# Kernel optimization log

Measured on AMD Instinct MI355X. Metric: run time of the kernel, lower is better.

Reference implementation:

```python
import jax, jax.numpy as jnp
import numpy as np

EMBED_DIM = 1024


def setup_inputs() -> dict:
    key = jax.random.key(0)
    ks = jax.random.split(key, 9)
    B, S, D = 4, 4096, EMBED_DIM
    s = 1.0 / np.sqrt(D)
    inp = {"x": jax.random.normal(ks[0], (B, S, D), dtype=jnp.float32)}
    names = ["q", "k", "v", "out"]
    for i, n in enumerate(names):
        inp[f"w_{n}"] = jax.random.uniform(ks[1 + 2 * i], (D, D), jnp.float32, -s, s)
        inp[f"b_{n}"] = jax.random.uniform(ks[2 + 2 * i], (D,), jnp.float32, -s, s)
    return inp


def reference(x, w_q, b_q, w_k, b_k, w_v, b_v, w_out, b_out):
    D = x.shape[-1]
    scaling = 1.0 / jnp.sqrt(jnp.asarray(D, x.dtype))
    q = jnp.einsum("bsd,ed->bse", x, w_q) + b_q
    k = jnp.einsum("bsd,ed->bse", x, w_k) + b_k
    v = jnp.einsum("bsd,ed->bse", x, w_v) + b_v
    # full [B, S, S] attention matrix, as in the original module
    scores = jnp.einsum("bqd,bkd->bqk", q, k) * scaling
    attn = jax.nn.softmax(scores, axis=-1)
    out = jnp.einsum("bqk,bkd->bqd", attn, v)
    return jnp.einsum("bsd,ed->bse", out, w_out) + b_out
```

## Files before the change

kernel.cpp:

```cpp
#include <hip/hip_runtime.h>
#include <hip/hip_bf16.h>

typedef __hip_bfloat16 bf16;
typedef __bf16 bf16x8 __attribute__((ext_vector_type(8)));
typedef float f32x4 __attribute__((ext_vector_type(4)));

#define B_ 4
#define S_ 4096
#define D_ 1024
#define BS_ 16384
#define N3_ 3072

__device__ __forceinline__ void gld_lds16(const void* g, void* l) {
    __builtin_amdgcn_global_load_lds(
        (const __attribute__((address_space(1))) void*)g,
        (__attribute__((address_space(3))) void*)l, 16, 0, 0);
}

__device__ __forceinline__ void cast4_one(const float* __restrict__ in,
                                          bf16* __restrict__ out, int i) {
    float4 v = ((const float4*)in)[i];
    union { ushort4 u; bf16 h[4]; } cv;
    cv.h[0] = __float2bfloat16(v.x);
    cv.h[1] = __float2bfloat16(v.y);
    cv.h[2] = __float2bfloat16(v.z);
    cv.h[3] = __float2bfloat16(v.w);
    ((ushort4*)out)[i] = cv.u;
}

__global__ __launch_bounds__(256) void prologue(
    const float* __restrict__ x, const float* __restrict__ wq,
    const float* __restrict__ wk, const float* __restrict__ wv,
    const float* __restrict__ wo, const float* __restrict__ bq,
    const float* __restrict__ bk, const float* __restrict__ bv,
    bf16* __restrict__ xb, bf16* __restrict__ Wc, bf16* __restrict__ Wo,
    float* __restrict__ bc, float* __restrict__ ls) {
    const int blk = blockIdx.x, tid = threadIdx.x;
    if (blk < 16384) {
        cast4_one(x, xb, blk * 256 + tid);
    } else if (blk < 20480) {
        int w = (blk - 16384) >> 10;
        int i = ((blk - 16384) & 1023) * 256 + tid;
        const float* src = (w == 0) ? wq : (w == 1) ? wk : (w == 2) ? wv : wo;
        bf16* dst = (w == 3) ? Wo : Wc + (long)w * D_ * D_;
        cast4_one(src, dst, i);
    } else if (blk < 20544) {
        ls[(blk - 20480) * 256 + tid] = 0.f;
    } else {
        for (int i = tid; i < N3_; i += 256)
            bc[i] = (i < 1024) ? bq[i] : (i < 2048) ? bk[i - 1024] : bv[i - 2048];
    }
}

__global__ __launch_bounds__(256) void transpose_v(const bf16* __restrict__ QKV,
                                                   bf16* __restrict__ VT) {
    __shared__ bf16 t[32][33];
    const int b = blockIdx.z;
    const bf16* Vb = QKV + (long)b * S_ * N3_ + 2048;
    bf16* VTb = VT + (long)b * D_ * S_;
    const int s0 = blockIdx.x * 32, d0 = blockIdx.y * 32;
    const int r = threadIdx.x >> 5, c = threadIdx.x & 31;
#pragma unroll
    for (int i = 0; i < 4; i++)
        t[r + i * 8][c] = Vb[(long)(s0 + r + i * 8) * N3_ + d0 + c];
    __syncthreads();
#pragma unroll
    for (int i = 0; i < 4; i++)
        VTb[(long)(d0 + r + i * 8) * S_ + s0 + c] = t[c][r + i * 8];
}

template <int EPI, int BM>
__global__ __launch_bounds__(256, 2) void gemm_nt(
    const bf16* __restrict__ A, int lda, long sA,
    const bf16* __restrict__ B, int ldb, long sB,
    void* __restrict__ Cout, int ldc, long sC,
    int K, const float* __restrict__ bias,
    float* __restrict__ rowsum, int sL, float scale) {
    constexpr int MI = BM / 32;
    __shared__ __align__(16) bf16 As[BM * 64];
    __shared__ __align__(16) bf16 Bs[128 * 64];
    const int tid = threadIdx.x;
    const int lane = tid & 63;
    const int wave = tid >> 6;
    const int bz = blockIdx.z;
    const int m0 = blockIdx.x * BM, n0 = blockIdx.y * 128;
    A += (long)bz * sA;
    B += (long)bz * sB;
    rowsum += (long)bz * sL;

    const int wr = (wave >> 1) * (BM / 2);
    const int wc = (wave & 1) * 64;
    const int fm = lane & 15;
    const int q4 = lane >> 4;
    const int sw = fm & 7;
    const int rd0 = ((q4 ^ sw) << 3);
    const int rd1 = (((4 + q4) ^ sw) << 3);

    f32x4 zero = {0.f, 0.f, 0.f, 0.f};
    f32x4 acc[MI][4];
#pragma unroll
    for (int i = 0; i < MI; i++)
#pragma unroll
        for (int j = 0; j < 4; j++) acc[i][j] = zero;

    for (int k0 = 0; k0 < K; k0 += 64) {
#pragma unroll
        for (int t = 0; t < BM / 32; t++) {
            int c = tid + t * 256;
            int row = c >> 3;
            int q = (((c & 7) ^ (row & 7)) << 3);
            gld_lds16(A + (long)(m0 + row) * lda + k0 + q, As + c * 8);
        }
#pragma unroll
        for (int t = 0; t < 4; t++) {
            int c = tid + t * 256;
            int row = c >> 3;
            int q = (((c & 7) ^ (row & 7)) << 3);
            gld_lds16(B + (long)(n0 + row) * ldb + k0 + q, Bs + c * 8);
        }
        __syncthreads();
#pragma unroll
        for (int kh = 0; kh < 2; kh++) {
            const int rdo = kh ? rd1 : rd0;
            bf16x8 af[MI], bfr[4];
#pragma unroll
            for (int i = 0; i < MI; i++)
                af[i] = *(const bf16x8*)(As + (wr + i * 16 + fm) * 64 + rdo);
#pragma unroll
            for (int j = 0; j < 4; j++)
                bfr[j] = *(const bf16x8*)(Bs + (wc + j * 16 + fm) * 64 + rdo);
#pragma unroll
            for (int i = 0; i < MI; i++)
#pragma unroll
                for (int j = 0; j < 4; j++)
                    acc[i][j] = __builtin_amdgcn_mfma_f32_16x16x32_bf16(
                        af[i], bfr[j], acc[i][j], 0, 0, 0);
        }
        __syncthreads();
    }

#pragma unroll
    for (int i = 0; i < MI; i++)
#pragma unroll
        for (int r = 0; r < 4; r++) {
            const int grow = m0 + wr + q4 * 4 + i * 16 + r;
            if constexpr (EPI == 0) {
#pragma unroll
                for (int j = 0; j < 4; j++) {
                    int gcol = n0 + wc + j * 16 + fm;
                    ((bf16*)Cout)[(long)bz * sC + (long)grow * ldc + gcol] =
                        __float2bfloat16(acc[i][j][r] + bias[gcol]);
                }
            } else if constexpr (EPI == 1) {
                float s = 0.f;
#pragma unroll
                for (int j = 0; j < 4; j++) {
                    int gcol = n0 + wc + j * 16 + fm;
                    float v = __expf(acc[i][j][r] * scale);
                    bf16 hv = __float2bfloat16(v);
                    ((bf16*)Cout)[(long)bz * sC + (long)grow * ldc + gcol] = hv;
                    s += __bfloat162float(hv);
                }
                s += __shfl_xor(s, 1, 16);
                s += __shfl_xor(s, 2, 16);
                s += __shfl_xor(s, 4, 16);
                s += __shfl_xor(s, 8, 16);
                if (fm == 0) atomicAdd(rowsum + grow, s);
            } else if constexpr (EPI == 2) {
                float inv = 1.0f / rowsum[grow];
#pragma unroll
                for (int j = 0; j < 4; j++) {
                    int gcol = n0 + wc + j * 16 + fm;
                    ((bf16*)Cout)[(long)bz * sC + (long)grow * ldc + gcol] =
                        __float2bfloat16(acc[i][j][r] * inv);
                }
            } else {
#pragma unroll
                for (int j = 0; j < 4; j++) {
                    int gcol = n0 + wc + j * 16 + fm;
                    ((float*)Cout)[(long)bz * sC + (long)grow * ldc + gcol] =
                        acc[i][j][r] + bias[gcol];
                }
            }
        }
}

extern "C" void kernel_launch(void* const* d_in, const int* in_sizes, int n_in,
                              void* d_out, int out_size, void* d_ws, size_t ws_size,
                              hipStream_t stream) {
    const float* x  = (const float*)d_in[0];
    const float* wq = (const float*)d_in[1];
    const float* bq = (const float*)d_in[2];
    const float* wk = (const float*)d_in[3];
    const float* bk = (const float*)d_in[4];
    const float* wv = (const float*)d_in[5];
    const float* bv = (const float*)d_in[6];
    const float* wo = (const float*)d_in[7];
    const float* bo = (const float*)d_in[8];
    (void)in_sizes; (void)n_in; (void)out_size;

    char* p = (char*)d_ws;
    bf16* Wc  = (bf16*)p;  p += (long)N3_ * D_ * 2;
    bf16* Wo  = (bf16*)p;  p += (long)D_ * D_ * 2;
    float* bc = (float*)p; p += N3_ * 4;
    bf16* QKV = (bf16*)p;  p += (long)BS_ * N3_ * 2;
    float* ls = (float*)p; p += (long)BS_ * 4;

    bf16* xb = (bf16*)d_out;

    const size_t base = 109129728UL;
    int tier;
    bf16 *VT, *E;
    if (ws_size >= base + 134217728UL) {
        tier = 2;
        E  = (bf16*)p;
        VT = (bf16*)((char*)d_out + 33554432);
    } else if (ws_size >= base + 33554432UL) {
        tier = 1;
        VT = (bf16*)p;
        E  = (bf16*)d_out;
    } else {
        tier = 0;
        VT = (bf16*)((char*)d_out + 33554432);
        E  = (bf16*)d_out;
    }

    prologue<<<dim3(20545), 256, 0, stream>>>(x, wq, wk, wv, wo, bq, bk, bv,
                                              xb, Wc, Wo, bc, ls);

    gemm_nt<0, 128><<<dim3(BS_ / 128, N3_ / 128, 1), 256, 0, stream>>>(
        xb, D_, 0, Wc, D_, 0, QKV, N3_, 0, D_, bc, ls, 0, 1.f);

    transpose_v<<<dim3(S_ / 32, D_ / 32, B_), 256, 0, stream>>>(QKV, VT);

    if (tier == 2) {
        gemm_nt<1, 128><<<dim3(32, 32, 4), 256, 0, stream>>>(
            QKV, N3_, (long)S_ * N3_, QKV + 1024, N3_, (long)S_ * N3_,
            E, S_, (long)S_ * S_, D_, nullptr, ls, S_, 0.03125f);
        gemm_nt<2, 128><<<dim3(32, 8, 4), 256, 0, stream>>>(
            E, S_, (long)S_ * S_, VT, S_, (long)D_ * S_,
            QKV, N3_, (long)S_ * N3_, S_, nullptr, ls, S_, 1.f);
    } else if (tier == 1) {
        for (int pr = 0; pr < 2; ++pr) {
            const long qoff = (long)(2 * pr) * S_ * N3_;
            gemm_nt<1, 128><<<dim3(32, 32, 2), 256, 0, stream>>>(
                QKV + qoff, N3_, (long)S_ * N3_,
                QKV + qoff + 1024, N3_, (long)S_ * N3_,
                E, S_, (long)S_ * S_, D_, nullptr, ls + 2 * pr * S_, S_, 0.03125f);
            gemm_nt<2, 128><<<dim3(32, 8, 2), 256, 0, stream>>>(
                E, S_, (long)S_ * S_,
                VT + (long)(2 * pr) * D_ * S_, S_, (long)D_ * S_,
                QKV + qoff, N3_, (long)S_ * N3_, S_, nullptr, ls + 2 * pr * S_, S_, 1.f);
        }
    } else {
        for (int b = 0; b < B_; ++b) {
            const long qoff = (long)b * S_ * N3_;
            gemm_nt<1, 128><<<dim3(32, 32, 1), 256, 0, stream>>>(
                QKV + qoff, N3_, 0, QKV + qoff + 1024, N3_, 0,
                E, S_, 0, D_, nullptr, ls + b * S_, 0, 0.03125f);
            gemm_nt<2, 64><<<dim3(64, 8, 1), 256, 0, stream>>>(
                E, S_, 0, VT + (long)b * D_ * S_, S_, 0,
                QKV + qoff, N3_, 0, S_, nullptr, ls + b * S_, 0, 1.f);
        }
    }

    gemm_nt<3, 128><<<dim3(BS_ / 128, D_ / 128, 1), 256, 0, stream>>>(
        QKV, N3_, 0, Wo, D_, 0, d_out, D_, 0, D_, bo, ls, 0, 1.f);
}
```

Before: 589.4 us.

## Add 256x256-tile 8-wave GEMM with ping-pong LDS pipeline for all matmuls

Introduces a new GEMM kernel with 256x256 output tiles, 512 threads (8 waves), double-buffered LDS fed by direct global-to-LDS loads, and interleaved barriers with MFMA priority raising, similar to a ping-pong schedule. The QKV projection, the scores/exp GEMM, the PV GEMM (tier 2 path) and the output projection are switched to it. The larger tile raises arithmetic intensity per LDS/global load and is meant to overlap loads with MFMA work. In exchange it uses 128KB of LDS and heavy register pressure, launches fewer blocks (wave-quantization risk), and the tier 0/1 fallback paths still use the old kernel.

```diff
diff --git a/kernel.cpp b/kernel.cpp
--- a/kernel.cpp
+++ b/kernel.cpp
@@ -185,6 +185,182 @@
         }
 }
 
+__device__ __forceinline__ void stage_half(const bf16* __restrict__ g, int ld,
+                                           bf16* l, int tid) {
+#pragma unroll
+    for (int t = 0; t < 2; t++) {
+        const int ch = tid + t * 512;
+        gld_lds16(g + (long)(ch >> 2) * ld + ((ch & 3) << 3), l + ch * 8);
+    }
+    asm volatile("" ::: "memory");
+}
+
+__device__ __forceinline__ void ds_a4(bf16x8 (&d)[4], const bf16* base, int ro,
+                                      int wr, int fm, int q4) {
+#pragma unroll
+    for (int i = 0; i < 4; i++)
+        d[i] = *(const bf16x8*)(base + (wr + ro + i * 16 + fm) * 32 + (q4 << 3));
+}
+
+__device__ __forceinline__ void ds_b4(bf16x8 (&d)[4], const bf16* base,
+                                      int wc, int fm, int q4) {
+#pragma unroll
+    for (int j = 0; j < 4; j++)
+        d[j] = *(const bf16x8*)(base + (wc + j * 16 + fm) * 32 + (q4 << 3));
+}
+
+template <int IO>
+__device__ __forceinline__ void mfma16(f32x4 (&acc)[8][4], const bf16x8 (&a)[4],
+                                       const bf16x8 (&b)[4]) {
+    __builtin_amdgcn_s_setprio(1);
+#pragma unroll
+    for (int i = 0; i < 4; i++)
+#pragma unroll
+        for (int j = 0; j < 4; j++)
+            acc[IO + i][j] = __builtin_amdgcn_mfma_f32_16x16x32_bf16(
+                a[i], b[j], acc[IO + i][j], 0, 0, 0);
+    __builtin_amdgcn_s_setprio(0);
+}
+
+#define BAR() __builtin_amdgcn_s_barrier()
+#define LGKM0() asm volatile("s_waitcnt lgkmcnt(0)" ::: "memory")
+#define VM4() asm volatile("s_waitcnt vmcnt(4)" ::: "memory")
+#define VM0() asm volatile("s_waitcnt vmcnt(0)" ::: "memory")
+
+template <int EPI>
+__global__ __launch_bounds__(512, 2) void gemm8(
+    const bf16* __restrict__ A, int lda, long sA,
+    const bf16* __restrict__ B, int ldb, long sB,
+    void* __restrict__ Cout, int ldc, long sC,
+    int K, const float* __restrict__ bias,
+    float* __restrict__ rowsum, int sL, float scale) {
+    __shared__ __align__(16) bf16 As[2][2][256 * 32];
+    __shared__ __align__(16) bf16 Bs[2][2][256 * 32];
+    const int tid = threadIdx.x;
+    const int lane = tid & 63;
+    const int wave = tid >> 6;
+    const int bz = blockIdx.z;
+    const int m0 = blockIdx.x * 256, n0 = blockIdx.y * 256;
+    A += (long)bz * sA + (long)m0 * lda;
+    B += (long)bz * sB + (long)n0 * ldb;
+    rowsum += (long)bz * sL;
+
+    const int wm = wave >> 2, wn = wave & 3;
+    const int wr = wm * 128, wc = wn * 64;
+    const int fm = lane & 15, q4 = lane >> 4;
+
+    f32x4 zero = {0.f, 0.f, 0.f, 0.f};
+    f32x4 acc[8][4];
+#pragma unroll
+    for (int i = 0; i < 8; i++)
+#pragma unroll
+        for (int j = 0; j < 4; j++) acc[i][j] = zero;
+
+    const int NT = K >> 6;
+    stage_half(A, lda, &As[0][0][0], tid);
+    stage_half(B, ldb, &Bs[0][0][0], tid);
+    stage_half(A + 32, lda, &As[0][1][0], tid);
+    stage_half(B + 32, ldb, &Bs[0][1][0], tid);
+    VM4();
+    BAR();
+
+    bf16x8 a[4], b[4];
+    for (int t = 0; t + 1 < NT; ++t) {
+        const int c = t & 1, n = c ^ 1;
+        const int kn = (t + 1) << 6;
+        ds_a4(a, &As[c][0][0], 0, wr, fm, q4);
+        ds_b4(b, &Bs[c][0][0], wc, fm, q4);
+        stage_half(A + kn, lda, &As[n][0][0], tid);
+        BAR(); LGKM0();
+        mfma16<0>(acc, a, b);
+        BAR();
+        ds_a4(a, &As[c][0][0], 64, wr, fm, q4);
+        stage_half(B + kn, ldb, &Bs[n][0][0], tid);
+        BAR(); LGKM0();
+        mfma16<4>(acc, a, b);
+        VM4();
+        BAR();
+        ds_a4(a, &As[c][1][0], 0, wr, fm, q4);
+        ds_b4(b, &Bs[c][1][0], wc, fm, q4);
+        stage_half(A + kn + 32, lda, &As[n][1][0], tid);
+        BAR(); LGKM0();
+        mfma16<0>(acc, a, b);
+        BAR();
+        ds_a4(a, &As[c][1][0], 64, wr, fm, q4);
+        stage_half(B + kn + 32, ldb, &Bs[n][1][0], tid);
+        BAR(); LGKM0();
+        mfma16<4>(acc, a, b);
+        VM4();
+        BAR();
+    }
+    {
+        const int c = (NT - 1) & 1;
+        ds_a4(a, &As[c][0][0], 0, wr, fm, q4);
+        ds_b4(b, &Bs[c][0][0], wc, fm, q4);
+        BAR(); LGKM0();
+        mfma16<0>(acc, a, b);
+        BAR();
+        ds_a4(a, &As[c][0][0], 64, wr, fm, q4);
+        BAR(); LGKM0();
+        mfma16<4>(acc, a, b);
+        VM0();
+        BAR();
+        ds_a4(a, &As[c][1][0], 0, wr, fm, q4);
+        ds_b4(b, &Bs[c][1][0], wc, fm, q4);
+        BAR(); LGKM0();
+        mfma16<0>(acc, a, b);
+        BAR();
+        ds_a4(a, &As[c][1][0], 64, wr, fm, q4);
+        BAR(); LGKM0();
+        mfma16<4>(acc, a, b);
+    }
+
+#pragma unroll
+    for (int mi = 0; mi < 8; mi++)
+#pragma unroll
+        for (int r = 0; r < 4; r++) {
+            const int grow = m0 + wr + mi * 16 + q4 * 4 + r;
+            if constexpr (EPI == 0) {
+#pragma unroll
+                for (int j = 0; j < 4; j++) {
+                    int gcol = n0 + wc + j * 16 + fm;
+                    ((bf16*)Cout)[(long)bz * sC + (long)grow * ldc + gcol] =
+                        __float2bfloat16(acc[mi][j][r] + bias[gcol]);
+                }
+            } else if constexpr (EPI == 1) {
+                float s = 0.f;
+#pragma unroll
+                for (int j = 0; j < 4; j++) {
+                    int gcol = n0 + wc + j * 16 + fm;
+                    float v = __expf(acc[mi][j][r] * scale);
+                    bf16 hv = __float2bfloat16(v);
+                    ((bf16*)Cout)[(long)bz * sC + (long)grow * ldc + gcol] = hv;
+                    s += __bfloat162float(hv);
+                }
+                s += __shfl_xor(s, 1, 16);
+                s += __shfl_xor(s, 2, 16);
+                s += __shfl_xor(s, 4, 16);
+                s += __shfl_xor(s, 8, 16);
+                if (fm == 0) atomicAdd(rowsum + grow, s);
+            } else if constexpr (EPI == 2) {
+                float inv = 1.0f / rowsum[grow];
+#pragma unroll
+                for (int j = 0; j < 4; j++) {
+                    int gcol = n0 + wc + j * 16 + fm;
+                    ((bf16*)Cout)[(long)bz * sC + (long)grow * ldc + gcol] =
+                        __float2bfloat16(acc[mi][j][r] * inv);
+                }
+            } else {
+#pragma unroll
+                for (int j = 0; j < 4; j++) {
+                    int gcol = n0 + wc + j * 16 + fm;
+                    ((float*)Cout)[(long)bz * sC + (long)grow * ldc + gcol] =
+                        acc[mi][j][r] + bias[gcol];
+                }
+            }
+        }
+}
+
 extern "C" void kernel_launch(void* const* d_in, const int* in_sizes, int n_in,
                               void* d_out, int out_size, void* d_ws, size_t ws_size,
                               hipStream_t stream) {
@@ -228,16 +404,16 @@
     prologue<<<dim3(20545), 256, 0, stream>>>(x, wq, wk, wv, wo, bq, bk, bv,
                                               xb, Wc, Wo, bc, ls);
 
-    gemm_nt<0, 128><<<dim3(BS_ / 128, N3_ / 128, 1), 256, 0, stream>>>(
+    gemm8<0><<<dim3(BS_ / 256, N3_ / 256, 1), 512, 0, stream>>>(
         xb, D_, 0, Wc, D_, 0, QKV, N3_, 0, D_, bc, ls, 0, 1.f);
 
     transpose_v<<<dim3(S_ / 32, D_ / 32, B_), 256, 0, stream>>>(QKV, VT);
 
     if (tier == 2) {
-        gemm_nt<1, 128><<<dim3(32, 32, 4), 256, 0, stream>>>(
+        gemm8<1><<<dim3(16, 16, 4), 512, 0, stream>>>(
             QKV, N3_, (long)S_ * N3_, QKV + 1024, N3_, (long)S_ * N3_,
             E, S_, (long)S_ * S_, D_, nullptr, ls, S_, 0.03125f);
-        gemm_nt<2, 128><<<dim3(32, 8, 4), 256, 0, stream>>>(
+        gemm8<2><<<dim3(16, 4, 4), 512, 0, stream>>>(
             E, S_, (long)S_ * S_, VT, S_, (long)D_ * S_,
             QKV, N3_, (long)S_ * N3_, S_, nullptr, ls, S_, 1.f);
     } else if (tier == 1) {
@@ -264,6 +440,6 @@
         }
     }
 
-    gemm_nt<3, 128><<<dim3(BS_ / 128, D_ / 128, 1), 256, 0, stream>>>(
+    gemm8<3><<<dim3(BS_ / 256, D_ / 256, 1), 512, 0, stream>>>(
         QKV, N3_, 0, Wo, D_, 0, d_out, D_, 0, D_, bo, ls, 0, 1.f);
 }
```

After: 707.0 us. 19.9% more time.

## Fuse V transpose into the QK^T score GEMM launch as extra blocks

Applied to the files above, without the earlier changes.

For the largest workspace tier, the separate transpose_v kernel is removed. The score GEMM grid gains an extra column of blocks (blockIdx.y == 32) that transposes V into VT with 16-byte vector loads and stores through a shared-memory union. This saves one kernel launch and lets the transpose overlap with the score GEMM blocks. The transpose blocks are small in count and do serial work, so they could become a tail in the grid.

```diff
diff --git a/kernel.cpp b/kernel.cpp
--- a/kernel.cpp
+++ b/kernel.cpp
@@ -75,10 +75,45 @@
     const bf16* __restrict__ B, int ldb, long sB,
     void* __restrict__ Cout, int ldc, long sC,
     int K, const float* __restrict__ bias,
-    float* __restrict__ rowsum, int sL, float scale) {
+    float* __restrict__ rowsum, int sL, float scale,
+    bf16* __restrict__ vt) {
+    union __align__(16) SMem {
+        struct { bf16 As[BM * 64]; bf16 Bs[128 * 64]; } g;
+        bf16 T[8][32][40];
+    };
+    __shared__ SMem sm;
+
+    if constexpr (EPI == 1) {
+        if (blockIdx.y == 32) {
+            const int bz2 = blockIdx.z;
+            const bf16* Vb = A + (long)bz2 * sA + 2048;
+            bf16* VTb = vt + (long)bz2 * D_ * S_;
+            const int tile = threadIdx.x >> 5, t32 = threadIdx.x & 31;
+            for (int it = 0; it < 16; ++it) {
+                const int ti = it * 8 + tile;
+                const int s0 = blockIdx.x * 128 + (ti & 3) * 32;
+                const int d0 = (ti >> 2) * 32;
+#pragma unroll
+                for (int c = 0; c < 4; ++c)
+                    *(bf16x8*)&sm.T[tile][t32][c * 8] =
+                        *(const bf16x8*)(Vb + (long)(s0 + t32) * N3_ + d0 + c * 8);
+                __syncthreads();
+                union { bf16x8 v[4]; bf16 h[32]; } col;
+#pragma unroll
+                for (int s = 0; s < 32; ++s) col.h[s] = sm.T[tile][s][t32];
+#pragma unroll
+                for (int c = 0; c < 4; ++c)
+                    *(bf16x8*)(VTb + (long)(d0 + t32) * S_ + s0 + c * 8) = col.v[c];
+                __syncthreads();
+            }
+            return;
+        }
+    }
+    (void)vt;
+
     constexpr int MI = BM / 32;
-    __shared__ __align__(16) bf16 As[BM * 64];
-    __shared__ __align__(16) bf16 Bs[128 * 64];
+    bf16* __restrict__ As = sm.g.As;
+    bf16* __restrict__ Bs = sm.g.Bs;
     const int tid = threadIdx.x;
     const int lane = tid & 63;
     const int wave = tid >> 6;
@@ -229,41 +264,41 @@
                                               xb, Wc, Wo, bc, ls);
 
     gemm_nt<0, 128><<<dim3(BS_ / 128, N3_ / 128, 1), 256, 0, stream>>>(
-        xb, D_, 0, Wc, D_, 0, QKV, N3_, 0, D_, bc, ls, 0, 1.f);
-
-    transpose_v<<<dim3(S_ / 32, D_ / 32, B_), 256, 0, stream>>>(QKV, VT);
+        xb, D_, 0, Wc, D_, 0, QKV, N3_, 0, D_, bc, ls, 0, 1.f, nullptr);
 
     if (tier == 2) {
-        gemm_nt<1, 128><<<dim3(32, 32, 4), 256, 0, stream>>>(
+        gemm_nt<1, 128><<<dim3(32, 33, 4), 256, 0, stream>>>(
             QKV, N3_, (long)S_ * N3_, QKV + 1024, N3_, (long)S_ * N3_,
-            E, S_, (long)S_ * S_, D_, nullptr, ls, S_, 0.03125f);
+            E, S_, (long)S_ * S_, D_, nullptr, ls, S_, 0.03125f, VT);
         gemm_nt<2, 128><<<dim3(32, 8, 4), 256, 0, stream>>>(
             E, S_, (long)S_ * S_, VT, S_, (long)D_ * S_,
-            QKV, N3_, (long)S_ * N3_, S_, nullptr, ls, S_, 1.f);
+            QKV, N3_, (long)S_ * N3_, S_, nullptr, ls, S_, 1.f, nullptr);
     } else if (tier == 1) {
+        transpose_v<<<dim3(S_ / 32, D_ / 32, B_), 256, 0, stream>>>(QKV, VT);
         for (int pr = 0; pr < 2; ++pr) {
             const long qoff = (long)(2 * pr) * S_ * N3_;
             gemm_nt<1, 128><<<dim3(32, 32, 2), 256, 0, stream>>>(
                 QKV + qoff, N3_, (long)S_ * N3_,
                 QKV + qoff + 1024, N3_, (long)S_ * N3_,
-                E, S_, (long)S_ * S_, D_, nullptr, ls + 2 * pr * S_, S_, 0.03125f);
+                E, S_, (long)S_ * S_, D_, nullptr, ls + 2 * pr * S_, S_, 0.03125f, nullptr);
             gemm_nt<2, 128><<<dim3(32, 8, 2), 256, 0, stream>>>(
                 E, S_, (long)S_ * S_,
                 VT + (long)(2 * pr) * D_ * S_, S_, (long)D_ * S_,
-                QKV + qoff, N3_, (long)S_ * N3_, S_, nullptr, ls + 2 * pr * S_, S_, 1.f);
+                QKV + qoff, N3_, (long)S_ * N3_, S_, nullptr, ls + 2 * pr * S_, S_, 1.f, nullptr);
         }
     } else {
+        transpose_v<<<dim3(S_ / 32, D_ / 32, B_), 256, 0, stream>>>(QKV, VT);
         for (int b = 0; b < B_; ++b) {
             const long qoff = (long)b * S_ * N3_;
             gemm_nt<1, 128><<<dim3(32, 32, 1), 256, 0, stream>>>(
                 QKV + qoff, N3_, 0, QKV + qoff + 1024, N3_, 0,
-                E, S_, 0, D_, nullptr, ls + b * S_, 0, 0.03125f);
+                E, S_, 0, D_, nullptr, ls + b * S_, 0, 0.03125f, nullptr);
             gemm_nt<2, 64><<<dim3(64, 8, 1), 256, 0, stream>>>(
                 E, S_, 0, VT + (long)b * D_ * S_, S_, 0,
-                QKV + qoff, N3_, 0, S_, nullptr, ls + b * S_, 0, 1.f);
+                QKV + qoff, N3_, 0, S_, nullptr, ls + b * S_, 0, 1.f, nullptr);
         }
     }
 
     gemm_nt<3, 128><<<dim3(BS_ / 128, D_ / 128, 1), 256, 0, stream>>>(
-        QKV, N3_, 0, Wo, D_, 0, d_out, D_, 0, D_, bo, ls, 0, 1.f);
-}
+        QKV, N3_, 0, Wo, D_, 0, d_out, D_, 0, D_, bo, ls, 0, 1.f, nullptr);
+}
```

New measurement: 597.8 us. About the same (+1.4%).
